# Kernel optimization log

Measured on AMD Instinct MI355X. Metric: run time of the kernel, lower is better.

The kernel has to match this reference:

```python
import jax, jax.numpy as jnp
import numpy as np

N = 8192


def setup_inputs() -> dict:
    key = jax.random.key(0)
    k1, k2 = jax.random.split(key)
    X = jax.random.normal(k1, (N,), dtype=jnp.float32)
    X_hat = jax.random.normal(k2, (N,), dtype=jnp.float32)
    return {"X": X, "X_hat": X_hat}


def reference(X, X_hat):
    n = X.shape[0]
    # Faithful to the torch module: compare argsort indices (not ranks)
    # over the full i,j meshgrid ('ij' indexing == broadcasting below).
    a = jnp.argsort(X)        # [n] int
    b = jnp.argsort(X_hat)    # [n] int
    ai, aj = a[:, None], a[None, :]   # [n,1], [1,n]
    bi, bj = b[:, None], b[None, :]
    disordered = ((ai < aj) & (bi > bj)) | ((ai > aj) & (bi < bj))  # [n,n] bool
    ndisordered = jnp.sum(disordered)
    return ndisordered.astype(jnp.float32) / (n * (n - 1))
```

## Files before the change

kernel.cpp:

```cpp
#include <hip/hip_runtime.h>

#define KN 8192

__device__ __forceinline__ unsigned long long make_key(float x, int idx) {
    unsigned int u = __float_as_uint(x);
    u ^= (unsigned int)((int)u >> 31) | 0x80000000u;
    return ((unsigned long long)u << 13) | (unsigned int)idx;
}

constexpr int UT  = 1024;
constexpr int VC  = 128;
constexpr int NVT = KN / VC;

__global__ __launch_bounds__(256) void rank_partial(const float* __restrict__ X,
                                                    const float* __restrict__ Xh,
                                                    int* __restrict__ part) {
    int blk = blockIdx.x;
    int arr = blk & 1;
    int vt  = (blk >> 1) & (NVT - 1);
    int ut  = blk >> 7;
    const float* src = arr ? Xh : X;

    int tid = threadIdx.x;
    int u0 = ut * UT + tid;

    unsigned long long ku0 = make_key(src[u0],       u0);
    unsigned long long ku1 = make_key(src[u0 + 256], u0 + 256);
    unsigned long long ku2 = make_key(src[u0 + 512], u0 + 512);
    unsigned long long ku3 = make_key(src[u0 + 768], u0 + 768);

    __shared__ unsigned long long tile[VC];
    if (tid < VC) {
        int v = vt * VC + tid;
        tile[tid] = make_key(src[v], v);
    }
    __syncthreads();

    int c0 = 0, c1 = 0, c2 = 0, c3 = 0;
#pragma unroll 8
    for (int jj = 0; jj < VC; ++jj) {
        unsigned long long kv = tile[jj];
        c0 += (kv < ku0);
        c1 += (kv < ku1);
        c2 += (kv < ku2);
        c3 += (kv < ku3);
    }

    int base = (arr * NVT + vt) * KN + u0;
    part[base]       = c0;
    part[base + 256] = c1;
    part[base + 512] = c2;
    part[base + 768] = c3;
}

__global__ __launch_bounds__(256) void reduce_scatter(const int* __restrict__ part,
                                                      int* __restrict__ a,
                                                      int* __restrict__ b) {
    int t = blockIdx.x * 256 + threadIdx.x;
    int arr = t >> 13;
    int u   = t & (KN - 1);

    const int* p = part + (arr * NVT) * KN + u;
    int r = 0;
#pragma unroll 8
    for (int vt = 0; vt < NVT; ++vt) r += p[vt * KN];

    if (arr == 0) a[r] = u; else b[r] = u;
}

__global__ __launch_bounds__(256) void gather_e(const int* __restrict__ a,
                                                const int* __restrict__ b,
                                                int* __restrict__ e) {
    int i = blockIdx.x * 256 + threadIdx.x;
    e[a[i]] = b[i];
}

__global__ __launch_bounds__(256) void inv_count(const int* __restrict__ e,
                                                 int* __restrict__ inv_part) {
    constexpr int TS = 256;
    constexpr int T  = KN / TS;

    int blk = blockIdx.x;
    int p = 0, rem = blk;
    while (rem >= T - p) { rem -= T - p; ++p; }
    int q = p + rem;

    __shared__ int le[TS];
    __shared__ int wsum[4];
    int tid = threadIdx.x;

    int ek = e[p * TS + tid];
    le[tid] = e[q * TS + tid];
    __syncthreads();

    int cnt = 0;
    if (p == q) {
        for (int j = tid + 1; j < TS; ++j) cnt += (ek > le[j]);
    } else {
        const int4* le4 = (const int4*)le;
#pragma unroll 8
        for (int j4 = 0; j4 < TS / 4; ++j4) {
            int4 v = le4[j4];
            cnt += (ek > v.x) + (ek > v.y) + (ek > v.z) + (ek > v.w);
        }
    }

    for (int off = 32; off; off >>= 1) cnt += __shfl_down(cnt, off);
    if ((tid & 63) == 0) wsum[tid >> 6] = cnt;
    __syncthreads();
    if (tid == 0) inv_part[blk] = wsum[0] + wsum[1] + wsum[2] + wsum[3];
}

__global__ __launch_bounds__(256) void finalize_k(const int* __restrict__ inv_part,
                                                  float* __restrict__ out) {
    __shared__ int wsum[4];
    int tid = threadIdx.x;
    int cnt = 0;
    for (int i = tid; i < 528; i += 256) cnt += inv_part[i];
    for (int off = 32; off; off >>= 1) cnt += __shfl_down(cnt, off);
    if ((tid & 63) == 0) wsum[tid >> 6] = cnt;
    __syncthreads();
    if (tid == 0) {
        float D = (float)(wsum[0] + wsum[1] + wsum[2] + wsum[3]);
        out[0] = 2.0f * D / ((float)KN * (float)(KN - 1));
    }
}

extern "C" void kernel_launch(void* const* d_in, const int* in_sizes, int n_in,
                              void* d_out, int out_size, void* d_ws, size_t ws_size,
                              hipStream_t stream) {
    const float* X  = (const float*)d_in[0];
    const float* Xh = (const float*)d_in[1];

    char* ws = (char*)d_ws;
    int* part     = (int*)(ws);
    int* a        = (int*)(ws + 4194304);
    int* b        = (int*)(ws + 4227072);
    int* e        = (int*)(ws + 4259840);
    int* inv_part = (int*)(ws + 4292608);

    rank_partial  <<<dim3(1024), dim3(256), 0, stream>>>(X, Xh, part);
    reduce_scatter<<<dim3(64),   dim3(256), 0, stream>>>(part, a, b);
    gather_e      <<<dim3(32),   dim3(256), 0, stream>>>(a, b, e);
    inv_count     <<<dim3(528),  dim3(256), 0, stream>>>(e, inv_part);
    finalize_k    <<<dim3(1),    dim3(256), 0, stream>>>(inv_part, (float*)d_out);
}
```

Baseline: 77.69 us.

## Fuse inversion counting with direct pair comparison and atomic finalize; widen rank tiles

Drops the gather and finalize kernels. A new pair_count kernel compares (a,b) pairs directly over the full n×n grid. A 64-bit atomic counter with a last-block detector writes the final ratio, which cuts the pipeline from five launches to three. Rank tiles are widened to 256 keys with 128-bit shared loads, which halves the rank_partial grid and the partial-sum traffic. The trade-off is that pair_count now does the full n² comparisons instead of only the upper triangle, and the result depends on the atomic counter being reset inside reduce_scatter.

After: 81.54 us. 1.05x slower.

```diff
diff --git a/kernel.cpp b/kernel.cpp
--- a/kernel.cpp
+++ b/kernel.cpp
@@ -9,7 +9,7 @@
 }
 
 constexpr int UT  = 1024;
-constexpr int VC  = 128;
+constexpr int VC  = 256;
 constexpr int NVT = KN / VC;
 
 __global__ __launch_bounds__(256) void rank_partial(const float* __restrict__ X,
@@ -18,7 +18,7 @@
     int blk = blockIdx.x;
     int arr = blk & 1;
     int vt  = (blk >> 1) & (NVT - 1);
-    int ut  = blk >> 7;
+    int ut  = blk >> 6;
     const float* src = arr ? Xh : X;
 
     int tid = threadIdx.x;
@@ -29,21 +29,22 @@
     unsigned long long ku2 = make_key(src[u0 + 512], u0 + 512);
     unsigned long long ku3 = make_key(src[u0 + 768], u0 + 768);
 
-    __shared__ unsigned long long tile[VC];
-    if (tid < VC) {
+    __shared__ __align__(16) unsigned long long tile[VC];
+    {
         int v = vt * VC + tid;
         tile[tid] = make_key(src[v], v);
     }
     __syncthreads();
 
+    const ulonglong2* t2 = (const ulonglong2*)tile;
     int c0 = 0, c1 = 0, c2 = 0, c3 = 0;
 #pragma unroll 8
-    for (int jj = 0; jj < VC; ++jj) {
-        unsigned long long kv = tile[jj];
-        c0 += (kv < ku0);
-        c1 += (kv < ku1);
-        c2 += (kv < ku2);
-        c3 += (kv < ku3);
+    for (int j = 0; j < VC / 2; ++j) {
+        ulonglong2 kv = t2[j];
+        c0 += (kv.x < ku0) + (kv.y < ku0);
+        c1 += (kv.x < ku1) + (kv.y < ku1);
+        c2 += (kv.x < ku2) + (kv.y < ku2);
+        c3 += (kv.x < ku3) + (kv.y < ku3);
     }
 
     int base = (arr * NVT + vt) * KN + u0;
@@ -55,74 +56,67 @@
 
 __global__ __launch_bounds__(256) void reduce_scatter(const int* __restrict__ part,
                                                       int* __restrict__ a,
-                                                      int* __restrict__ b) {
+                                                      int* __restrict__ b,
+                                                      unsigned long long* __restrict__ acc) {
     int t = blockIdx.x * 256 + threadIdx.x;
+    if (t == 0) *acc = 0ULL;
     int arr = t >> 13;
     int u   = t & (KN - 1);
 
     const int* p = part + (arr * NVT) * KN + u;
     int r = 0;
-#pragma unroll 8
+#pragma unroll
     for (int vt = 0; vt < NVT; ++vt) r += p[vt * KN];
 
     if (arr == 0) a[r] = u; else b[r] = u;
 }
 
-__global__ __launch_bounds__(256) void gather_e(const int* __restrict__ a,
-                                                const int* __restrict__ b,
-                                                int* __restrict__ e) {
-    int i = blockIdx.x * 256 + threadIdx.x;
-    e[a[i]] = b[i];
-}
+constexpr int KT    = 1024;
+constexpr int LT    = 128;
+constexpr int NLT   = KN / LT;
+constexpr int NBLK3 = (KN / KT) * NLT;
 
-__global__ __launch_bounds__(256) void inv_count(const int* __restrict__ e,
-                                                 int* __restrict__ inv_part) {
-    constexpr int TS = 256;
-    constexpr int T  = KN / TS;
-
+__global__ __launch_bounds__(256) void pair_count(const int* __restrict__ a,
+                                                  const int* __restrict__ b,
+                                                  unsigned long long* __restrict__ acc,
+                                                  float* __restrict__ out) {
     int blk = blockIdx.x;
-    int p = 0, rem = blk;
-    while (rem >= T - p) { rem -= T - p; ++p; }
-    int q = p + rem;
-
-    __shared__ int le[TS];
-    __shared__ int wsum[4];
+    int lt  = blk & (NLT - 1);
+    int kt  = blk >> 6;
     int tid = threadIdx.x;
 
-    int ek = e[p * TS + tid];
-    le[tid] = e[q * TS + tid];
+    __shared__ int2 tl[LT];
+    __shared__ int wsum[4];
+    if (tid < LT) {
+        int l = lt * LT + tid;
+        tl[tid] = make_int2(a[l], b[l]);
+    }
+    int k0  = kt * KT + tid;
+    int ak0 = a[k0], ak1 = a[k0 + 256], ak2 = a[k0 + 512], ak3 = a[k0 + 768];
+    int bk0 = b[k0], bk1 = b[k0 + 256], bk2 = b[k0 + 512], bk3 = b[k0 + 768];
     __syncthreads();
 
-    int cnt = 0;
-    if (p == q) {
-        for (int j = tid + 1; j < TS; ++j) cnt += (ek > le[j]);
-    } else {
-        const int4* le4 = (const int4*)le;
+    int c = 0;
 #pragma unroll 8
-        for (int j4 = 0; j4 < TS / 4; ++j4) {
-            int4 v = le4[j4];
-            cnt += (ek > v.x) + (ek > v.y) + (ek > v.z) + (ek > v.w);
-        }
+    for (int j = 0; j < LT; ++j) {
+        int2 v = tl[j];
+        c += (ak0 < v.x) != (bk0 < v.y);
+        c += (ak1 < v.x) != (bk1 < v.y);
+        c += (ak2 < v.x) != (bk2 < v.y);
+        c += (ak3 < v.x) != (bk3 < v.y);
     }
 
-    for (int off = 32; off; off >>= 1) cnt += __shfl_down(cnt, off);
-    if ((tid & 63) == 0) wsum[tid >> 6] = cnt;
-    __syncthreads();
-    if (tid == 0) inv_part[blk] = wsum[0] + wsum[1] + wsum[2] + wsum[3];
-}
-
-__global__ __launch_bounds__(256) void finalize_k(const int* __restrict__ inv_part,
-                                                  float* __restrict__ out) {
-    __shared__ int wsum[4];
-    int tid = threadIdx.x;
-    int cnt = 0;
-    for (int i = tid; i < 528; i += 256) cnt += inv_part[i];
-    for (int off = 32; off; off >>= 1) cnt += __shfl_down(cnt, off);
-    if ((tid & 63) == 0) wsum[tid >> 6] = cnt;
+    for (int off = 32; off; off >>= 1) c += __shfl_down(c, off);
+    if ((tid & 63) == 0) wsum[tid >> 6] = c;
     __syncthreads();
     if (tid == 0) {
-        float D = (float)(wsum[0] + wsum[1] + wsum[2] + wsum[3]);
-        out[0] = 2.0f * D / ((float)KN * (float)(KN - 1));
+        unsigned long long partial =
+            (unsigned long long)(wsum[0] + wsum[1] + wsum[2] + wsum[3]);
+        unsigned long long old = atomicAdd(acc, (1ULL << 40) | partial);
+        if ((old >> 40) == (unsigned long long)(NBLK3 - 1)) {
+            unsigned long long total = (old & ((1ULL << 40) - 1)) + partial;
+            out[0] = (float)total / 67100672.0f;
+        }
     }
 }
 
@@ -133,15 +127,12 @@
     const float* Xh = (const float*)d_in[1];
 
     char* ws = (char*)d_ws;
-    int* part     = (int*)(ws);
-    int* a        = (int*)(ws + 4194304);
-    int* b        = (int*)(ws + 4227072);
-    int* e        = (int*)(ws + 4259840);
-    int* inv_part = (int*)(ws + 4292608);
+    int* part = (int*)(ws);
+    int* a    = (int*)(ws + 2097152);
+    int* b    = (int*)(ws + 2129920);
+    unsigned long long* acc = (unsigned long long*)(ws + 2162688);
 
-    rank_partial  <<<dim3(1024), dim3(256), 0, stream>>>(X, Xh, part);
-    reduce_scatter<<<dim3(64),   dim3(256), 0, stream>>>(part, a, b);
-    gather_e      <<<dim3(32),   dim3(256), 0, stream>>>(a, b, e);
-    inv_count     <<<dim3(528),  dim3(256), 0, stream>>>(e, inv_part);
-    finalize_k    <<<dim3(1),    dim3(256), 0, stream>>>(inv_part, (float*)d_out);
+    rank_partial  <<<dim3(512), dim3(256), 0, stream>>>(X, Xh, part);
+    reduce_scatter<<<dim3(64),  dim3(256), 0, stream>>>(part, a, b, acc);
+    pair_count    <<<dim3(512), dim3(256), 0, stream>>>(a, b, acc, (float*)d_out);
 }
```
